# Kernel optimization log

Hardware: AMD Instinct MI355X
Metric: run time of the kernel (lower is better)

The kernel has to match this reference:

```python
import jax, jax.numpy as jnp
import numpy as np

B, N_NODES, N_MEM, DEG, D, R = 64, 50000, 65536, 4, 128, 500
E = N_MEM * DEG


def _mlp2(x, W1, b1, W2, b2):
    # F layer with n_layers=2: Dense(leaky_relu) -> Dense(tanh); tf.nn.leaky_relu alpha=0.2
    h = jax.nn.leaky_relu(x @ W1 + b1, negative_slope=0.2)
    return jnp.tanh(h @ W2 + b2)


def setup_inputs() -> dict:
    key = jax.random.key(0)
    ks = jax.random.split(key, 17)
    eg_e = jax.random.randint(ks[0], (E,), 0, B)
    rel = jax.random.randint(ks[1], (E,), 0, R)
    e2vi = jax.random.randint(ks[2], (E,), 0, N_MEM)
    idx_vi = jax.random.randint(ks[3], (E,), 0, N_MEM)
    # every memorized node receives DEG edges; new_idx_e2vj == idx_vj (DPMPN invariant)
    idx_vj = jnp.tile(jnp.arange(N_MEM), DEG)
    z = jnp.zeros((E,), jnp.int32)
    seen_edges = jnp.stack([eg_e, z, z, rel, idx_vi, idx_vj, e2vi, idx_vj], axis=1).astype(jnp.int32)
    eg_m = jax.random.randint(ks[4], (N_MEM,), 0, B)
    v_m = jax.random.randint(ks[5], (N_MEM,), 0, N_NODES)
    memorized_nodes = jnp.stack([eg_m, v_m], axis=1).astype(jnp.int32)
    s = 0.05
    return {
        'hidden': jax.random.normal(ks[6], (N_MEM, D), jnp.float32),
        'seen_edges': seen_edges,
        'memorized_nodes': memorized_nodes,
        'node_attention': jax.random.uniform(ks[7], (B, N_NODES), jnp.float32),
        'hidden_uncon': jax.random.normal(ks[8], (1, N_NODES, D), jnp.float32),
        'query_head_emb': jax.random.normal(ks[9], (B, D), jnp.float32),
        'query_rel_emb': jax.random.normal(ks[10], (B, D), jnp.float32),
        'rel_table': jax.random.normal(ks[11], (R, D), jnp.float32),
        'msg_W1': jax.random.normal(ks[12], (5 * D, D), jnp.float32) * s,
        'msg_b1': jnp.zeros((D,), jnp.float32),
        'msg_W2': jax.random.normal(ks[13], (D, D), jnp.float32) * s,
        'msg_b2': jnp.zeros((D,), jnp.float32),
        'hid_W1': jax.random.normal(ks[14], (5 * D, D), jnp.float32) * s,
        'hid_b1': jnp.zeros((D,), jnp.float32),
        'hid_W2': jax.random.normal(ks[15], (D, D), jnp.float32) * s,
        'hid_b2': jnp.zeros((D,), jnp.float32),
        'int_W': jax.random.normal(ks[16], (D, D), jnp.float32) * s,
    }


def reference(hidden, seen_edges, memorized_nodes, node_attention, hidden_uncon,
              query_head_emb, query_rel_emb, rel_table,
              msg_W1, msg_b1, msg_W2, msg_b2,
              hid_W1, hid_b1, hid_W2, hid_b2, int_W):
    n_mem = hidden.shape[0]
    # node2edge: gather endpoint features to edges
    eg_e = seen_edges[:, 0]
    hidden_vi = hidden[seen_edges[:, 6]]
    hidden_vj = hidden[seen_edges[:, 7]]
    rel_emb = rel_table[seen_edges[:, 3]]
    qh_e = query_head_emb[eg_e]
    qr_e = query_rel_emb[eg_e]
    msg_in = jnp.concatenate([hidden_vi, rel_emb, hidden_vj, qh_e, qr_e], axis=-1)  # [E, 5D]
    message = _mlp2(msg_in, msg_W1, msg_b1, msg_W2, msg_b2)  # [E, D]
    # aggregate at vj, aggr_op 'mean_v3': unsorted_segment_mean * sqrt(count), then scatter
    idx_vj = seen_edges[:, 5]
    seg_sum = jax.ops.segment_sum(message, idx_vj, num_segments=n_mem)
    cnt = jax.ops.segment_sum(jnp.ones((E,), message.dtype), idx_vj, num_segments=n_mem)
    aggr = seg_sum * (jnp.sqrt(cnt) / jnp.maximum(cnt, 1.0))[:, None]
    red = jax.ops.segment_max(seen_edges[:, 7], idx_vj, num_segments=n_mem)
    nonempty = cnt > 0
    red = jnp.where(nonempty, red, 0)
    message_aggr = jnp.zeros_like(hidden).at[red].add(jnp.where(nonempty[:, None], aggr, 0.0))
    # unconscious-flow intervention per memorized node
    eg_m = memorized_nodes[:, 0]
    v_m = memorized_nodes[:, 1]
    hu = hidden_uncon[0][v_m]  # [n_mem, D]
    na = node_attention[eg_m, v_m]  # [n_mem]
    hu = (na[:, None] * hu) @ int_W
    qh_m = query_head_emb[eg_m]
    qr_m = query_rel_emb[eg_m]
    upd_in = jnp.concatenate([message_aggr, hidden, hu, qh_m, qr_m], axis=-1)  # [n_mem, 5D]
    update = _mlp2(upd_in, hid_W1, hid_b1, hid_W2, hid_b2)
    return hidden + update
```

## Files before the change

kernel.cpp:

```cpp
#include <hip/hip_runtime.h>
#include <hip/hip_bf16.h>

typedef unsigned short u16;
typedef __attribute__((ext_vector_type(8))) short bf16x8;
typedef __attribute__((ext_vector_type(4))) float f32x4;

#define N_MEM_C 65536
#define NNODES_C 50000
#define DDIM 128
#define BM 128
#define NTHR 512
#define TIL(t) ((t) * 16384)

__device__ __align__(16) u16 g_WT[7 * 16384];
__device__ __align__(16) float g_relW[500 * 128];
__device__ __align__(16) float g_qsumM[64 * 128];
__device__ __align__(16) float g_qsumH[64 * 128];
__device__ __align__(16) u16 g_hb[(size_t)N_MEM_C * DDIM];
__device__ __align__(16) u16 g_ub[(size_t)NNODES_C * DDIM];

#define SBAR() do { asm volatile("" ::: "memory"); __builtin_amdgcn_s_barrier(); \
                    asm volatile("" ::: "memory"); } while (0)
#define WAIT_VM0() asm volatile("s_waitcnt vmcnt(0)" ::: "memory")
#define WAIT_VM4() asm volatile("s_waitcnt vmcnt(4)" ::: "memory")
#define WAIT_LG0() asm volatile("s_waitcnt lgkmcnt(0)" ::: "memory")

__device__ __forceinline__ u16 f2bf_s(float f) {
  __hip_bfloat16 h = __float2bfloat16(f);
  u16 u; __builtin_memcpy(&u, &h, 2);
  return u;
}
__device__ __forceinline__ unsigned pk2(float a, float b) {
  __hip_bfloat162 h = __float22bfloat162_rn(make_float2(a, b));
  unsigned u; __builtin_memcpy(&u, &h, 4);
  return u;
}
__device__ __forceinline__ float bf2f(u16 u) {
  unsigned v = ((unsigned)u) << 16;
  float f; __builtin_memcpy(&f, &v, 4);
  return f;
}
__device__ __forceinline__ float fast_tanh(float x) {
  float e = __expf(2.0f * x);
  return 1.0f - 2.0f / (e + 1.0f);
}
__device__ __forceinline__ int swz_off(int r, int c) {
  return r * 128 + ((((c >> 3) ^ (r & 7)) << 3) | (c & 7));
}

extern "C" __global__ void prep_all(const float* __restrict__ hidden,
                                    const float* __restrict__ uncon,
                                    const float* __restrict__ msg_W1,
                                    const float* __restrict__ msg_W2,
                                    const float* __restrict__ hid_W1,
                                    const float* __restrict__ hid_W2,
                                    const float* __restrict__ int_W,
                                    const float* __restrict__ rel_table,
                                    const float* __restrict__ qh,
                                    const float* __restrict__ qr) {
  int bid = blockIdx.x;
  if (bid < 7221) {
    const size_t NH = (size_t)N_MEM_C * DDIM / 8;
    size_t i = (size_t)bid * 256 + threadIdx.x;
    const float* src; u16* dst; size_t o;
    if (i < NH) { src = hidden; dst = g_hb; o = i; }
    else { src = uncon; dst = g_ub; o = i - NH; }
    const float4* p = (const float4*)(src + o * 8);
    float4 a = p[0], b = p[1];
    *(uint4*)(dst + o * 8) =
        make_uint4(pk2(a.x, a.y), pk2(a.z, a.w), pk2(b.x, b.y), pk2(b.z, b.w));
  } else if (bid < 7605) {
    int i = (bid - 7221) * 256 + threadIdx.x;
    int t = i >> 14, idx = i & 16383;
    int n = idx >> 7, k = idx & 127;
    const float* src; int dst;
    switch (t) {
      case 0:  src = msg_W1;             dst = TIL(0); break;
      case 1:  src = msg_W1 + 256 * 128; dst = TIL(1); break;
      case 2:  src = msg_W2;             dst = TIL(2); break;
      case 3:  src = hid_W1;             dst = TIL(3); break;
      case 4:  src = hid_W1 + 128 * 128; dst = TIL(4); break;
      default: src = hid_W2;             dst = TIL(6); break;
    }
    g_WT[dst + swz_off(n, k)] = f2bf_s(src[k * 128 + n]);
  } else if (bid < 7669) {
    int i = (bid - 7605) * 256 + threadIdx.x;
    int n = i & 127, q = i >> 7;
    float s = 0.f;
    for (int p = 0; p < 128; ++p)
      s += int_W[q * 128 + p] * hid_W1[(256 + p) * 128 + n];
    g_WT[TIL(5) + swz_off(n, q)] = f2bf_s(s);
  } else if (bid < 7919) {
    int i = (bid - 7669) * 256 + threadIdx.x;
    int r = i >> 7, n = i & 127;
    float s = 0.f;
    for (int k = 0; k < 128; ++k)
      s += rel_table[r * 128 + k] * msg_W1[(128 + k) * 128 + n];
    g_relW[i] = s;
  } else {
    int i = (bid - 7919) * 256 + threadIdx.x;
    int g = i >> 7, n = i & 127;
    float sM = 0.f, sH = 0.f;
    for (int k = 0; k < 128; ++k) {
      float h = qh[g * 128 + k], r = qr[g * 128 + k];
      sM += h * msg_W1[(384 + k) * 128 + n] + r * msg_W1[(512 + k) * 128 + n];
      sH += h * hid_W1[(384 + k) * 128 + n] + r * hid_W1[(512 + k) * 128 + n];
    }
    g_qsumM[i] = sM;
    g_qsumH[i] = sH;
  }
}

__device__ __forceinline__ void gload_rows(u16* lds_tile, const u16* __restrict__ gsrc,
                                           const int* idxArr, int base,
                                           int wid, int lane) {
  int rsub = lane >> 4, s = lane & 15;
#pragma unroll
  for (int k = 0; k < 4; ++k) {
    int r = wid * 16 + k * 4 + rsub;
    int idx = idxArr ? idxArr[r] : (base + r);
    const u16* gp = gsrc + (size_t)idx * DDIM + ((s ^ (r & 7)) << 3);
    u16* lp = lds_tile + (wid * 16 + k * 4) * 128;
    __builtin_amdgcn_global_load_lds((const __attribute__((address_space(1))) void*)gp,
                                     (__attribute__((address_space(3))) void*)lp,
                                     16, 0, 0);
  }
}
__device__ __forceinline__ void gload_lin(u16* lds_tile, const u16* __restrict__ gsrc,
                                          int wid, int lane) {
#pragma unroll
  for (int k = 0; k < 4; ++k) {
    int off = (wid * 4 + k) * 512;
    const u16* gp = gsrc + off + lane * 8;
    u16* lp = lds_tile + off;
    __builtin_amdgcn_global_load_lds((const __attribute__((address_space(1))) void*)gp,
                                     (__attribute__((address_space(3))) void*)lp,
                                     16, 0, 0);
  }
}

__device__ __forceinline__ void gemmS(const u16* A, const u16* W,
                                      f32x4 (&acc)[4][2], int wr, int wc, int l16, int l4) {
#pragma unroll
  for (int ks = 0; ks < 4; ++ks) {
    int gsl = ks * 4 + l4;
    bf16x8 av[4], bv[2];
#pragma unroll
    for (int nr = 0; nr < 2; ++nr) {
      int rW = wc * 32 + nr * 16 + l16;
      bv[nr] = *(const bf16x8*)&W[rW * 128 + ((gsl ^ (rW & 7)) << 3)];
    }
#pragma unroll
    for (int mr = 0; mr < 4; ++mr) {
      int rA = wr * 64 + mr * 16 + l16;
      av[mr] = *(const bf16x8*)&A[rA * 128 + ((gsl ^ (rA & 7)) << 3)];
    }
#pragma unroll
    for (int mr = 0; mr < 4; ++mr)
#pragma unroll
      for (int nr = 0; nr < 2; ++nr)
        acc[mr][nr] = __builtin_amdgcn_mfma_f32_16x16x32_bf16(av[mr], bv[nr], acc[mr][nr], 0, 0, 0);
  }
}

extern "C" __global__ __launch_bounds__(NTHR, 2) void fused_flow(
    const int* __restrict__ seen_edges, const int* __restrict__ memorized,
    const float* __restrict__ node_att,
    const float* __restrict__ msg_b1, const float* __restrict__ msg_b2,
    const float* __restrict__ hid_b1, const float* __restrict__ hid_b2,
    float* __restrict__ out) {
  __shared__ u16 sA0[16384], sA1[16384];
  __shared__ u16 sW0b[16384], sW2b[16384];
  __shared__ int sEg[4][BM], sRel[4][BM], sVi[4][BM];
  __shared__ int sMeg[BM], sMvm[BM];
  __shared__ float sNA[BM];

  const int tid = threadIdx.x;
  const int lane = tid & 63, wid = tid >> 6;
  const int wr = wid >> 2, wc = wid & 3;
  const int l16 = lane & 15, l4 = lane >> 4;
  const int j0 = blockIdx.x * BM;

  float mb1v[2], mb2v[2], hb1v[2], hb2v[2];
#pragma unroll
  for (int nr = 0; nr < 2; ++nr) {
    int col = wc * 32 + nr * 16 + l16;
    mb1v[nr] = msg_b1[col]; mb2v[nr] = msg_b2[col];
    hb1v[nr] = hid_b1[col]; hb2v[nr] = hid_b2[col];
  }

  gload_lin(sW0b, g_WT + TIL(0), wid, lane);
  gload_lin(sW2b, g_WT + TIL(1), wid, lane);
  gload_rows(sA0, g_hb, nullptr, j0, wid, lane);
  {
    int t = tid >> 7, r = tid & 127;
    int e = j0 + r + t * N_MEM_C;
    const int4* se = (const int4*)seen_edges + (size_t)e * 2;
    int4 lo = se[0], hi = se[1];
    sEg[t][r] = min(max(lo.x, 0), 63);
    sRel[t][r] = min(max(lo.w, 0), 499);
    sVi[t][r] = min(max(hi.z, 0), N_MEM_C - 1);
  }
  if (tid < BM) {
    int2 mn = ((const int2*)memorized)[j0 + tid];
    int eg = min(max(mn.x, 0), 63);
    int vm = min(max(mn.y, 0), NNODES_C - 1);
    sMeg[tid] = eg; sMvm[tid] = vm;
    sNA[tid] = node_att[(size_t)eg * NNODES_C + vm];
  }
  WAIT_LG0(); SBAR();
  gload_rows(sA1, g_hb, sVi[0], 0, wid, lane);
  WAIT_VM0(); SBAR();

  const f32x4 zero4 = {0.f, 0.f, 0.f, 0.f};
  f32x4 acc_vj[4][2], aggr[4][2];
#pragma unroll
  for (int a = 0; a < 4; ++a)
#pragma unroll
    for (int b = 0; b < 2; ++b) { acc_vj[a][b] = zero4; aggr[a][b] = zero4; }
  gemmS(sA0, sW2b, acc_vj, wr, wc, l16, l4);
  SBAR();
  gload_lin(sW2b, g_WT + TIL(2), wid, lane);
  gload_rows(sA0, g_hb, sVi[1], 0, wid, lane);

#pragma unroll 1
  for (int t = 0; t < 4; ++t) {
    u16* Acur = (t & 1) ? sA0 : sA1;
    f32x4 acc[4][2];
#pragma unroll
    for (int a = 0; a < 4; ++a)
#pragma unroll
      for (int b = 0; b < 2; ++b) acc[a][b] = acc_vj[a][b];
    gemmS(Acur, sW0b, acc, wr, wc, l16, l4);

#pragma unroll
    for (int mr = 0; mr < 4; ++mr)
#pragma unroll
      for (int i = 0; i < 4; ++i) {
        int r = wr * 64 + mr * 16 + l4 * 4 + i;
        const float* pr = g_relW + sRel[t][r] * 128;
        const float* pq = g_qsumM + sEg[t][r] * 128;
#pragma unroll
        for (int nr = 0; nr < 2; ++nr) {
          int c = wc * 32 + nr * 16 + l16;
          acc[mr][nr][i] += pr[c] + pq[c];
        }
      }
    SBAR();

#pragma unroll
    for (int mr = 0; mr < 4; ++mr)
#pragma unroll
      for (int nr = 0; nr < 2; ++nr)
#pragma unroll
        for (int i = 0; i < 4; ++i) {
          float v = acc[mr][nr][i] + mb1v[nr];
          v = (v >= 0.f) ? v : 0.2f * v;
          int r = wr * 64 + mr * 16 + l4 * 4 + i;
          Acur[swz_off(r, wc * 32 + nr * 16 + l16)] = f2bf_s(v);
        }
    WAIT_LG0();
    if (t == 0) { WAIT_VM4(); }
    SBAR();

    f32x4 acc2[4][2];
#pragma unroll
    for (int a = 0; a < 4; ++a)
#pragma unroll
      for (int b = 0; b < 2; ++b) acc2[a][b] = zero4;
    gemmS(Acur, sW2b, acc2, wr, wc, l16, l4);
#pragma unroll
    for (int mr = 0; mr < 4; ++mr)
#pragma unroll
      for (int nr = 0; nr < 2; ++nr)
#pragma unroll
        for (int i = 0; i < 4; ++i)
          aggr[mr][nr][i] += fast_tanh(acc2[mr][nr][i] + mb2v[nr]);
    WAIT_VM0();
    SBAR();
    if (t < 2)
      gload_rows(Acur, g_hb, sVi[t + 2], 0, wid, lane);
  }

  gload_lin(sW0b, g_WT + TIL(3), wid, lane);
  gload_lin(sW2b, g_WT + TIL(4), wid, lane);
  gload_rows(sA0, g_hb, nullptr, j0, wid, lane);
#pragma unroll
  for (int mr = 0; mr < 4; ++mr)
#pragma unroll
    for (int nr = 0; nr < 2; ++nr)
#pragma unroll
      for (int i = 0; i < 4; ++i) {
        int r = wr * 64 + mr * 16 + l4 * 4 + i;
        sA1[swz_off(r, wc * 32 + nr * 16 + l16)] = f2bf_s(0.5f * aggr[mr][nr][i]);
      }
  WAIT_LG0(); WAIT_VM0(); SBAR();

  f32x4 accU[4][2];
#pragma unroll
  for (int a = 0; a < 4; ++a)
#pragma unroll
    for (int b = 0; b < 2; ++b) accU[a][b] = zero4;
  gemmS(sA1, sW0b, accU, wr, wc, l16, l4);
  SBAR();
  gload_lin(sW0b, g_WT + TIL(5), wid, lane);
  gload_rows(sA1, g_ub, sMvm, 0, wid, lane);
  gemmS(sA0, sW2b, accU, wr, wc, l16, l4);
  SBAR();
  gload_lin(sW2b, g_WT + TIL(6), wid, lane);
  WAIT_VM4(); SBAR();

  f32x4 acc2[4][2];
#pragma unroll
  for (int a = 0; a < 4; ++a)
#pragma unroll
    for (int b = 0; b < 2; ++b) acc2[a][b] = zero4;
  gemmS(sA1, sW0b, acc2, wr, wc, l16, l4);
#pragma unroll
  for (int mr = 0; mr < 4; ++mr)
#pragma unroll
    for (int i = 0; i < 4; ++i) {
      int r = wr * 64 + mr * 16 + l4 * 4 + i;
      float na = sNA[r];
      const float* pq = g_qsumH + sMeg[r] * 128;
#pragma unroll
      for (int nr = 0; nr < 2; ++nr)
        accU[mr][nr][i] += na * acc2[mr][nr][i] + pq[wc * 32 + nr * 16 + l16];
    }
#pragma unroll
  for (int mr = 0; mr < 4; ++mr)
#pragma unroll
    for (int nr = 0; nr < 2; ++nr)
#pragma unroll
      for (int i = 0; i < 4; ++i) {
        float v = accU[mr][nr][i] + hb1v[nr];
        v = (v >= 0.f) ? v : 0.2f * v;
        int r = wr * 64 + mr * 16 + l4 * 4 + i;
        sA0[swz_off(r, wc * 32 + nr * 16 + l16)] = f2bf_s(v);
      }
  WAIT_LG0(); WAIT_VM0(); SBAR();

  f32x4 accF[4][2];
#pragma unroll
  for (int a = 0; a < 4; ++a)
#pragma unroll
    for (int b = 0; b < 2; ++b) accF[a][b] = zero4;
  gemmS(sA0, sW2b, accF, wr, wc, l16, l4);

#pragma unroll
  for (int mr = 0; mr < 4; ++mr)
#pragma unroll
    for (int nr = 0; nr < 2; ++nr)
#pragma unroll
      for (int i = 0; i < 4; ++i) {
        int row = j0 + wr * 64 + mr * 16 + l4 * 4 + i;
        int col = wc * 32 + nr * 16 + l16;
        size_t o = (size_t)row * DDIM + col;
        out[o] = bf2f(g_hb[o]) + fast_tanh(accF[mr][nr][i] + hb2v[nr]);
      }
}

extern "C" void kernel_launch(void* const* d_in, const int* in_sizes, int n_in,
                              void* d_out, int out_size, void* d_ws, size_t ws_size,
                              hipStream_t stream) {
  (void)in_sizes; (void)n_in; (void)out_size; (void)d_ws; (void)ws_size;
  const float* hidden       = (const float*)d_in[0];
  const int*   seen_edges   = (const int*)d_in[1];
  const int*   memorized    = (const int*)d_in[2];
  const float* node_att     = (const float*)d_in[3];
  const float* hidden_uncon = (const float*)d_in[4];
  const float* qh           = (const float*)d_in[5];
  const float* qr           = (const float*)d_in[6];
  const float* rel_table    = (const float*)d_in[7];
  const float* msg_W1       = (const float*)d_in[8];
  const float* msg_b1       = (const float*)d_in[9];
  const float* msg_W2       = (const float*)d_in[10];
  const float* msg_b2       = (const float*)d_in[11];
  const float* hid_W1       = (const float*)d_in[12];
  const float* hid_b1       = (const float*)d_in[13];
  const float* hid_W2       = (const float*)d_in[14];
  const float* hid_b2       = (const float*)d_in[15];
  const float* int_W        = (const float*)d_in[16];

  prep_all<<<dim3(7951), dim3(256), 0, stream>>>(
      hidden, hidden_uncon, msg_W1, msg_W2, hid_W1, hid_W2, int_W,
      rel_table, qh, qr);
  fused_flow<<<dim3(N_MEM_C / BM), dim3(NTHR), 0, stream>>>(
      seen_edges, memorized, node_att, msg_b1, msg_b2, hid_b1, hid_b2, (float*)d_out);
}
```

Baseline: 117.5 us.

## Read transposed weight tiles from global/L2 instead of staging them in LDS

The weight tiles are now stored unswizzled, row-major and transposed in global memory. The GEMM helper reads B fragments straight from global memory (L1/L2) rather than from LDS copies. This drops the two 32KB LDS weight buffers and the matching async loads and waits, which cuts LDS use per block and removes several barrier and wait points. The helper also raises wave priority around the MFMA loop. The cost is that every weight fragment becomes a global load with higher latency inside the GEMM inner loop.

```diff
diff --git a/kernel.cpp b/kernel.cpp
--- a/kernel.cpp
+++ b/kernel.cpp
@@ -22,7 +22,6 @@
 #define SBAR() do { asm volatile("" ::: "memory"); __builtin_amdgcn_s_barrier(); \
                     asm volatile("" ::: "memory"); } while (0)
 #define WAIT_VM0() asm volatile("s_waitcnt vmcnt(0)" ::: "memory")
-#define WAIT_VM4() asm volatile("s_waitcnt vmcnt(4)" ::: "memory")
 #define WAIT_LG0() asm volatile("s_waitcnt lgkmcnt(0)" ::: "memory")
 
 __device__ __forceinline__ u16 f2bf_s(float f) {
@@ -82,14 +81,14 @@
       case 4:  src = hid_W1 + 128 * 128; dst = TIL(4); break;
       default: src = hid_W2;             dst = TIL(6); break;
     }
-    g_WT[dst + swz_off(n, k)] = f2bf_s(src[k * 128 + n]);
+    g_WT[dst + n * 128 + k] = f2bf_s(src[k * 128 + n]);
   } else if (bid < 7669) {
     int i = (bid - 7605) * 256 + threadIdx.x;
     int n = i & 127, q = i >> 7;
     float s = 0.f;
     for (int p = 0; p < 128; ++p)
       s += int_W[q * 128 + p] * hid_W1[(256 + p) * 128 + n];
-    g_WT[TIL(5) + swz_off(n, q)] = f2bf_s(s);
+    g_WT[TIL(5) + n * 128 + q] = f2bf_s(s);
   } else if (bid < 7919) {
     int i = (bid - 7669) * 256 + threadIdx.x;
     int r = i >> 7, n = i & 127;
@@ -126,30 +125,18 @@
                                      16, 0, 0);
   }
 }
-__device__ __forceinline__ void gload_lin(u16* lds_tile, const u16* __restrict__ gsrc,
-                                          int wid, int lane) {
-#pragma unroll
-  for (int k = 0; k < 4; ++k) {
-    int off = (wid * 4 + k) * 512;
-    const u16* gp = gsrc + off + lane * 8;
-    u16* lp = lds_tile + off;
-    __builtin_amdgcn_global_load_lds((const __attribute__((address_space(1))) void*)gp,
-                                     (__attribute__((address_space(3))) void*)lp,
-                                     16, 0, 0);
-  }
-}
-
-__device__ __forceinline__ void gemmS(const u16* A, const u16* W,
+
+__device__ __forceinline__ void gemmG(const u16* A, const u16* __restrict__ WT,
                                       f32x4 (&acc)[4][2], int wr, int wc, int l16, int l4) {
+  const u16* wb = WT + (wc * 32 + l16) * 128 + l4 * 8;
+  __builtin_amdgcn_s_setprio(1);
 #pragma unroll
   for (int ks = 0; ks < 4; ++ks) {
     int gsl = ks * 4 + l4;
     bf16x8 av[4], bv[2];
 #pragma unroll
-    for (int nr = 0; nr < 2; ++nr) {
-      int rW = wc * 32 + nr * 16 + l16;
-      bv[nr] = *(const bf16x8*)&W[rW * 128 + ((gsl ^ (rW & 7)) << 3)];
-    }
+    for (int nr = 0; nr < 2; ++nr)
+      bv[nr] = *(const bf16x8*)(wb + nr * 16 * 128 + ks * 32);
 #pragma unroll
     for (int mr = 0; mr < 4; ++mr) {
       int rA = wr * 64 + mr * 16 + l16;
@@ -161,6 +148,7 @@
       for (int nr = 0; nr < 2; ++nr)
         acc[mr][nr] = __builtin_amdgcn_mfma_f32_16x16x32_bf16(av[mr], bv[nr], acc[mr][nr], 0, 0, 0);
   }
+  __builtin_amdgcn_s_setprio(0);
 }
 
 extern "C" __global__ __launch_bounds__(NTHR, 2) void fused_flow(
@@ -170,7 +158,6 @@
     const float* __restrict__ hid_b1, const float* __restrict__ hid_b2,
     float* __restrict__ out) {
   __shared__ u16 sA0[16384], sA1[16384];
-  __shared__ u16 sW0b[16384], sW2b[16384];
   __shared__ int sEg[4][BM], sRel[4][BM], sVi[4][BM];
   __shared__ int sMeg[BM], sMvm[BM];
   __shared__ float sNA[BM];
@@ -189,8 +176,6 @@
     hb1v[nr] = hid_b1[col]; hb2v[nr] = hid_b2[col];
   }
 
-  gload_lin(sW0b, g_WT + TIL(0), wid, lane);
-  gload_lin(sW2b, g_WT + TIL(1), wid, lane);
   gload_rows(sA0, g_hb, nullptr, j0, wid, lane);
   {
     int t = tid >> 7, r = tid & 127;
@@ -218,9 +203,8 @@
   for (int a = 0; a < 4; ++a)
 #pragma unroll
     for (int b = 0; b < 2; ++b) { acc_vj[a][b] = zero4; aggr[a][b] = zero4; }
-  gemmS(sA0, sW2b, acc_vj, wr, wc, l16, l4);
+  gemmG(sA0, g_WT + TIL(1), acc_vj, wr, wc, l16, l4);
   SBAR();
-  gload_lin(sW2b, g_WT + TIL(2), wid, lane);
   gload_rows(sA0, g_hb, sVi[1], 0, wid, lane);
 
 #pragma unroll 1
@@ -231,7 +215,7 @@
     for (int a = 0; a < 4; ++a)
 #pragma unroll
       for (int b = 0; b < 2; ++b) acc[a][b] = acc_vj[a][b];
-    gemmS(Acur, sW0b, acc, wr, wc, l16, l4);
+    gemmG(Acur, g_WT + TIL(0), acc, wr, wc, l16, l4);
 
 #pragma unroll
     for (int mr = 0; mr < 4; ++mr)
@@ -259,16 +243,14 @@
           int r = wr * 64 + mr * 16 + l4 * 4 + i;
           Acur[swz_off(r, wc * 32 + nr * 16 + l16)] = f2bf_s(v);
         }
-    WAIT_LG0();
-    if (t == 0) { WAIT_VM4(); }
-    SBAR();
+    WAIT_LG0(); SBAR();
 
     f32x4 acc2[4][2];
 #pragma unroll
     for (int a = 0; a < 4; ++a)
 #pragma unroll
       for (int b = 0; b < 2; ++b) acc2[a][b] = zero4;
-    gemmS(Acur, sW2b, acc2, wr, wc, l16, l4);
+    gemmG(Acur, g_WT + TIL(2), acc2, wr, wc, l16, l4);
 #pragma unroll
     for (int mr = 0; mr < 4; ++mr)
 #pragma unroll
@@ -282,8 +264,6 @@
       gload_rows(Acur, g_hb, sVi[t + 2], 0, wid, lane);
   }
 
-  gload_lin(sW0b, g_WT + TIL(3), wid, lane);
-  gload_lin(sW2b, g_WT + TIL(4), wid, lane);
   gload_rows(sA0, g_hb, nullptr, j0, wid, lane);
 #pragma unroll
   for (int mr = 0; mr < 4; ++mr)
@@ -301,21 +281,18 @@
   for (int a = 0; a < 4; ++a)
 #pragma unroll
     for (int b = 0; b < 2; ++b) accU[a][b] = zero4;
-  gemmS(sA1, sW0b, accU, wr, wc, l16, l4);
+  gemmG(sA1, g_WT + TIL(3), accU, wr, wc, l16, l4);
+  gemmG(sA0, g_WT + TIL(4), accU, wr, wc, l16, l4);
   SBAR();
-  gload_lin(sW0b, g_WT + TIL(5), wid, lane);
   gload_rows(sA1, g_ub, sMvm, 0, wid, lane);
-  gemmS(sA0, sW2b, accU, wr, wc, l16, l4);
-  SBAR();
-  gload_lin(sW2b, g_WT + TIL(6), wid, lane);
-  WAIT_VM4(); SBAR();
+  WAIT_VM0(); SBAR();
 
   f32x4 acc2[4][2];
 #pragma unroll
   for (int a = 0; a < 4; ++a)
 #pragma unroll
     for (int b = 0; b < 2; ++b) acc2[a][b] = zero4;
-  gemmS(sA1, sW0b, acc2, wr, wc, l16, l4);
+  gemmG(sA1, g_WT + TIL(5), acc2, wr, wc, l16, l4);
 #pragma unroll
   for (int mr = 0; mr < 4; ++mr)
 #pragma unroll
@@ -338,14 +315,14 @@
         int r = wr * 64 + mr * 16 + l4 * 4 + i;
         sA0[swz_off(r, wc * 32 + nr * 16 + l16)] = f2bf_s(v);
       }
-  WAIT_LG0(); WAIT_VM0(); SBAR();
+  WAIT_LG0(); SBAR();
 
   f32x4 accF[4][2];
 #pragma unroll
   for (int a = 0; a < 4; ++a)
 #pragma unroll
     for (int b = 0; b < 2; ++b) accF[a][b] = zero4;
-  gemmS(sA0, sW2b, accF, wr, wc, l16, l4);
+  gemmG(sA0, g_WT + TIL(6), accF, wr, wc, l16, l4);
 
 #pragma unroll
   for (int mr = 0; mr < 4; ++mr)
```

Result: slower. 149.8 us (+27.5%).
